# Performance work log

Hardware: AMD Instinct MI355X
Metric: run time of the kernel (lower is better)

Reference implementation:

```python
import jax, jax.numpy as jnp
import numpy as np

N, E, F_IN, EDIM, H = 50000, 1600000, 128, 16, 4
C1, C2, G, NCLS = 32, 8, 64, 10
NEG_SLOPE = 0.2


def setup_inputs() -> dict:
    key = jax.random.key(0)
    ks = jax.random.split(key, 20)
    s = 0.1
    inp = {
        "x": jax.random.normal(ks[0], (N, F_IN), jnp.float32),
        "edge_index": jax.random.randint(ks[1], (2, E), 0, N, dtype=jnp.int32),
        "edge_attr": jax.random.normal(ks[2], (E, EDIM), jnp.float32),
        "batch": jnp.sort(jax.random.randint(ks[3], (N,), 0, G, dtype=jnp.int32)),
        # layer 1 params (PyG GATConv: shared lin for src/dst, no lin bias)
        "W1": jax.random.normal(ks[4], (F_IN, H * C1), jnp.float32) * s,
        "as1": jax.random.normal(ks[5], (H, C1), jnp.float32) * s,
        "ad1": jax.random.normal(ks[6], (H, C1), jnp.float32) * s,
        "We1": jax.random.normal(ks[7], (EDIM, H * C1), jnp.float32) * s,
        "ae1": jax.random.normal(ks[8], (H, C1), jnp.float32) * s,
        "b1": jnp.zeros((H * C1,), jnp.float32),
        # layer 2 params
        "W2": jax.random.normal(ks[9], (H * C1, H * C2), jnp.float32) * s,
        "as2": jax.random.normal(ks[10], (H, C2), jnp.float32) * s,
        "ad2": jax.random.normal(ks[11], (H, C2), jnp.float32) * s,
        "We2": jax.random.normal(ks[12], (EDIM, H * C2), jnp.float32) * s,
        "ae2": jax.random.normal(ks[13], (H, C2), jnp.float32) * s,
        "b2": jnp.zeros((H * C2,), jnp.float32),
        # final linear
        "Wfc": jax.random.normal(ks[14], (H * C2, NCLS), jnp.float32) * s,
        "bfc": jnp.zeros((NCLS,), jnp.float32),
    }
    return inp


def _add_self_loops(src, dst, edge_attr):
    # PyG default: add_self_loops=True, fill_value='mean' (mean of incoming edge attrs)
    deg = jax.ops.segment_sum(jnp.ones((E,), jnp.float32), dst, num_segments=N)
    loop_attr = jax.ops.segment_sum(edge_attr, dst, num_segments=N) / jnp.maximum(deg, 1.0)[:, None]
    loop = jnp.arange(N, dtype=src.dtype)
    return (jnp.concatenate([src, loop]), jnp.concatenate([dst, loop]),
            jnp.concatenate([edge_attr, loop_attr], axis=0))


def _gat_layer(x, src, dst, ea, W, a_src, a_dst, We, a_e, b, heads, ch):
    n = x.shape[0]
    h = (x @ W).reshape(n, heads, ch)                 # [N,H,C]
    he = (ea @ We).reshape(-1, heads, ch)             # [Ef,H,C]
    al_src = jnp.einsum('nhc,hc->nh', h, a_src)       # [N,H]
    al_dst = jnp.einsum('nhc,hc->nh', h, a_dst)
    al_e = jnp.einsum('ehc,hc->eh', he, a_e)          # [Ef,H]
    alpha = al_src[src] + al_dst[dst] + al_e
    alpha = jax.nn.leaky_relu(alpha, NEG_SLOPE)
    # edge softmax grouped by destination node
    amax = jax.ops.segment_max(alpha, dst, num_segments=n)
    alpha = jnp.exp(alpha - amax[dst])
    denom = jax.ops.segment_sum(alpha, dst, num_segments=n)
    alpha = alpha / (denom[dst] + 1e-16)
    out = jax.ops.segment_sum(h[src] * alpha[..., None], dst, num_segments=n)  # [N,H,C]
    return out.reshape(n, heads * ch) + b


def reference(x, edge_index, edge_attr, batch, W1, as1, ad1, We1, ae1, b1,
              W2, as2, ad2, We2, ae2, b2, Wfc, bfc):
    src, dst = edge_index[0], edge_index[1]
    src, dst, ea = _add_self_loops(src, dst, edge_attr)
    h = jax.nn.relu(_gat_layer(x, src, dst, ea, W1, as1, ad1, We1, ae1, b1, H, C1))
    h = jax.nn.relu(_gat_layer(h, src, dst, ea, W2, as2, ad2, We2, ae2, b2, H, C2))
    # global mean pool over graphs
    cnt = jax.ops.segment_sum(jnp.ones((N,), jnp.float32), batch, num_segments=G)
    pooled = jax.ops.segment_sum(h, batch, num_segments=G) / jnp.maximum(cnt, 1.0)[:, None]
    return pooled @ Wfc + bfc
```

## Files before the change

kernel.cpp:

```cpp
#include <hip/hip_runtime.h>
#include <hip/hip_fp16.h>
#include <math.h>

typedef float4 f4;
#define NEG_SLOPE 0.2f
#define NBMAX 1024
#define BIN_CHUNK 8192

union h4pack { float2 f; __half2 h[2]; };

__global__ void k_prep(const float* __restrict__ We1, const float* __restrict__ ae1,
                       const float* __restrict__ We2, const float* __restrict__ ae2,
                       float* __restrict__ M) {
    int t = threadIdx.x;
    if (t >= 128) return;
    int sel = t >> 6, i = t & 63, d = i >> 2, h = i & 3;
    const float* W  = sel ? We2 : We1;
    const float* ae = sel ? ae2 : ae1;
    int C = sel ? 8 : 32, ncol = sel ? 32 : 128;
    float s = 0.f;
    for (int c = 0; c < C; ++c) s += W[d * ncol + h * C + c] * ae[h * C + c];
    M[sel * 64 + d * 4 + h] = s;
}

__global__ __launch_bounds__(256) void k_bhist(const int* __restrict__ ei,
                                               int* __restrict__ bcnt, int E, int NB) {
    __shared__ int hist[NBMAX];
    for (int i = threadIdx.x; i < NB; i += 256) hist[i] = 0;
    __syncthreads();
    int stride = gridDim.x * 256;
    for (int e = blockIdx.x * 256 + threadIdx.x; e < E; e += stride)
        atomicAdd(&hist[ei[E + e] >> 6], 1);
    __syncthreads();
    for (int i = threadIdx.x; i < NB; i += 256) {
        int h = hist[i];
        if (h) atomicAdd(&bcnt[i], h);
    }
}

__global__ void k_bscan(const int* __restrict__ bcnt, int* __restrict__ bprefix,
                        int* __restrict__ bcursor, int NB) {
    __shared__ int ts[NBMAX];
    int t = threadIdx.x;
    ts[t] = (t < NB) ? bcnt[t] : 0;
    __syncthreads();
    for (int off = 1; off < 1024; off <<= 1) {
        int v = (t >= off) ? ts[t - off] : 0;
        __syncthreads();
        ts[t] += v;
        __syncthreads();
    }
    int excl = (t == 0) ? 0 : ts[t - 1];
    if (t <= NB) {
        bprefix[t] = excl;
        if (t < NB) bcursor[t] = excl;
    }
}

__global__ void k_ale_lin(const float* __restrict__ ea, const float* __restrict__ Mbuf,
                          __half* __restrict__ ale1_e, __half* __restrict__ ale2_e, int E) {
    __shared__ float Ms[128];
    if (threadIdx.x < 128) Ms[threadIdx.x] = Mbuf[threadIdx.x];
    __syncthreads();
    int e = blockIdx.x * 256 + threadIdx.x;
    if (e >= E) return;
    const f4* row = (const f4*)(ea + (size_t)e * 16);
    f4 r0 = row[0], r1 = row[1], r2 = row[2], r3 = row[3];
    float a[16] = { r0.x, r0.y, r0.z, r0.w, r1.x, r1.y, r1.z, r1.w,
                    r2.x, r2.y, r2.z, r2.w, r3.x, r3.y, r3.z, r3.w };
    float s10 = 0.f, s11 = 0.f, s12 = 0.f, s13 = 0.f;
    float s20 = 0.f, s21 = 0.f, s22 = 0.f, s23 = 0.f;
#pragma unroll
    for (int dd = 0; dd < 16; ++dd) {
        float av = a[dd];
        s10 += av * Ms[dd * 4 + 0]; s11 += av * Ms[dd * 4 + 1];
        s12 += av * Ms[dd * 4 + 2]; s13 += av * Ms[dd * 4 + 3];
        s20 += av * Ms[64 + dd * 4 + 0]; s21 += av * Ms[64 + dd * 4 + 1];
        s22 += av * Ms[64 + dd * 4 + 2]; s23 += av * Ms[64 + dd * 4 + 3];
    }
    h4pack p1, p2;
    p1.h[0] = __floats2half2_rn(s10, s11); p1.h[1] = __floats2half2_rn(s12, s13);
    p2.h[0] = __floats2half2_rn(s20, s21); p2.h[1] = __floats2half2_rn(s22, s23);
    ((float2*)ale1_e)[e] = p1.f;
    ((float2*)ale2_e)[e] = p2.f;
}

__global__ __launch_bounds__(256) void k_bin(const int* __restrict__ ei,
                                             int* __restrict__ bcursor,
                                             int2* __restrict__ binned, int E, int NB) {
    __shared__ int hist[NBMAX], base[NBMAX], cur[NBMAX];
    for (int i = threadIdx.x; i < NB; i += 256) { hist[i] = 0; cur[i] = 0; }
    __syncthreads();
    int e0 = blockIdx.x * BIN_CHUNK;
    int e1 = min(e0 + BIN_CHUNK, E);
    for (int e = e0 + threadIdx.x; e < e1; e += 256)
        atomicAdd(&hist[ei[E + e] >> 6], 1);
    __syncthreads();
    for (int i = threadIdx.x; i < NB; i += 256) {
        int h = hist[i];
        if (h) base[i] = atomicAdd(&bcursor[i], h);
    }
    __syncthreads();
    for (int e = e0 + threadIdx.x; e < e1; e += 256) {
        int sr = ei[e], d = ei[E + e];
        int b = d >> 6;
        int loc = base[b] + atomicAdd(&cur[b], 1);
        binned[loc] = make_int2(sr, ((d & 63) << 26) | e);
    }
}

__global__ __launch_bounds__(256) void k_csr(const int2* __restrict__ binned,
                                             const float2* __restrict__ ale1_e,
                                             const float2* __restrict__ ale2_e,
                                             const int* __restrict__ bprefix,
                                             int* __restrict__ offsets,
                                             int* __restrict__ csr_src,
                                             float2* __restrict__ csr_ale1,
                                             float2* __restrict__ csr_ale2,
                                             int N, int E, int NB) {
    __shared__ int nhist[64], noff[65];
    int b = blockIdx.x;
    if (threadIdx.x < 64) nhist[threadIdx.x] = 0;
    __syncthreads();
    int lo = bprefix[b], hi = bprefix[b + 1];
    for (int s = lo + threadIdx.x; s < hi; s += 256)
        atomicAdd(&nhist[(binned[s].y >> 26) & 63], 1);
    __syncthreads();
    if (threadIdx.x == 0) {
        int run = 0;
        for (int i = 0; i < 64; ++i) { noff[i] = run; run += nhist[i]; }
        noff[64] = run;
    }
    __syncthreads();
    int nlo = b << 6;
    int nbn = min(64, N - nlo);
    if (threadIdx.x < nbn) offsets[nlo + threadIdx.x] = lo + noff[threadIdx.x];
    if (b == NB - 1 && threadIdx.x == 0) offsets[N] = E;
    if (threadIdx.x < 64) nhist[threadIdx.x] = 0;
    __syncthreads();
    for (int s = lo + threadIdx.x; s < hi; s += 256) {
        int2 r = binned[s];
        int dl = (r.y >> 26) & 63;
        int eid = r.y & 0x03FFFFFF;
        float2 a1 = ale1_e[eid];
        float2 a2 = ale2_e[eid];
        int slot = lo + noff[dl] + atomicAdd(&nhist[dl], 1);
        csr_src[slot] = r.x;
        csr_ale1[slot] = a1;
        csr_ale2[slot] = a2;
    }
}

template<int NOUT, int ROWS>
__global__ __launch_bounds__(256) void k_gemm(const float* __restrict__ X,
                                              const float* __restrict__ W,
                                              __half* __restrict__ Hout, int N) {
    __shared__ __align__(16) float xs[ROWS][128];
    int row0 = blockIdx.x * ROWS;
    int tid = threadIdx.x;
    constexpr int NF4 = ROWS * 32;
    const f4* x4 = (const f4*)X;
    for (int i = tid; i < NF4; i += 256) {
        int r = i >> 5, k4 = i & 31;
        f4 v;
        if (row0 + r < N) v = x4[(size_t)(row0 + r) * 32 + k4];
        else { v.x = v.y = v.z = v.w = 0.f; }
        ((f4*)&xs[r][0])[k4] = v;
    }
    __syncthreads();
    constexpr int GRP = 256 / NOUT;
    constexpr int PR  = ROWS / GRP;
    int col = tid % NOUT, rg = tid / NOUT;
    float acc[PR];
#pragma unroll
    for (int r = 0; r < PR; ++r) acc[r] = 0.f;
    for (int k = 0; k < 128; ++k) {
        float w = W[k * NOUT + col];
#pragma unroll
        for (int r = 0; r < PR; ++r) acc[r] += xs[rg + r * GRP][k] * w;
    }
#pragma unroll
    for (int r = 0; r < PR; ++r) {
        int row = row0 + rg + r * GRP;
        if (row < N) Hout[(size_t)row * NOUT + col] = __float2half(acc[r]);
    }
}

template<int C>
__global__ void k_al(const __half* __restrict__ Hm, const float* __restrict__ as_,
                     const float* __restrict__ ad_, float* __restrict__ als,
                     float* __restrict__ ald, int N) {
    int idx = blockIdx.x * 256 + threadIdx.x;
    int n = idx >> 2, h = idx & 3;
    if (n >= N) return;
    constexpr int CH = C / 4;
    const __half2* h2p = (const __half2*)(Hm + (size_t)n * C + h * CH);
    float a = 0.f, b = 0.f;
#pragma unroll
    for (int c = 0; c < CH / 2; ++c) {
        float2 v = __half22float2(h2p[c]);
        a += v.x * as_[h * CH + 2 * c] + v.y * as_[h * CH + 2 * c + 1];
        b += v.x * ad_[h * CH + 2 * c] + v.y * ad_[h * CH + 2 * c + 1];
    }
    als[n * 4 + h] = a;
    ald[n * 4 + h] = b;
}

__global__ __launch_bounds__(256) void k_alpha_node(const float2* __restrict__ csr_ale,
                                                    __half* __restrict__ alpha_csr,
                                                    const int* __restrict__ csr_src,
                                                    const float* __restrict__ als,
                                                    const float* __restrict__ ald,
                                                    const int* __restrict__ offsets,
                                                    float* __restrict__ rden,
                                                    float* __restrict__ selfa, int N) {
    int n = (blockIdx.x * 256 + threadIdx.x) >> 6;
    int lane = threadIdx.x & 63;
    if (n >= N) return;
    int j = lane >> 2, h = lane & 3;
    int s0 = offsets[n], s1 = offsets[n + 1];
    float aldn = ald[n * 4 + h];
    float den = 0.f, asum = 0.f;
    const __half* aleh = (const __half*)csr_ale;
    for (int base = s0; base < s1; base += 16) {
        int s = base + j;
        if (s < s1) {
            int src = csr_src[s];
            float ale = __half2float(aleh[(size_t)s * 4 + h]);
            float v = als[src * 4 + h] + aldn + ale;
            v = (v > 0.f) ? v : NEG_SLOPE * v;
            float e = __expf(v);
            alpha_csr[s * 4 + h] = __float2half(e);
            den += e; asum += ale;
        }
    }
    den  += __shfl_xor(den, 4);  den  += __shfl_xor(den, 8);
    den  += __shfl_xor(den, 16); den  += __shfl_xor(den, 32);
    asum += __shfl_xor(asum, 4);  asum += __shfl_xor(asum, 8);
    asum += __shfl_xor(asum, 16); asum += __shfl_xor(asum, 32);
    if (j == 0) {
        float rdeg = 1.f / fmaxf((float)(s1 - s0), 1.f);
        float v = als[n * 4 + h] + aldn + asum * rdeg;
        v = (v > 0.f) ? v : NEG_SLOPE * v;
        float es = __expf(v);
        selfa[n * 4 + h] = es;
        rden[n * 4 + h] = 1.f / (den + es + 1e-16f);
    }
}

__global__ __launch_bounds__(256) void k_aggf128(const __half* __restrict__ h16,
                                                 const __half* __restrict__ alpha16,
                                                 const float* __restrict__ rden,
                                                 const float* __restrict__ selfa,
                                                 const int* __restrict__ offsets,
                                                 const int* __restrict__ csr_src,
                                                 const float* __restrict__ bias,
                                                 float* __restrict__ Out, int N) {
    int n = (blockIdx.x * 256 + threadIdx.x) >> 6;
    int lane = threadIdx.x & 63;
    if (n >= N) return;
    int hd = lane >> 4;
    int s0 = offsets[n], s1 = offsets[n + 1];
    const __half2* H2 = (const __half2*)h16;
    float acc0 = 0.f, acc1 = 0.f;
    int e1 = s1 - 1;
    for (int s = s0; s < s1; s += 8) {
        int srck[8]; float ak[8]; __half2 hvk[8];
#pragma unroll
        for (int k = 0; k < 8; ++k) {
            int sk = min(s + k, e1);
            srck[k] = csr_src[sk];
            ak[k] = (s + k <= e1) ? __half2float(alpha16[(size_t)sk * 4 + hd]) : 0.f;
        }
#pragma unroll
        for (int k = 0; k < 8; ++k) hvk[k] = H2[(size_t)srck[k] * 64 + lane];
#pragma unroll
        for (int k = 0; k < 8; ++k) {
            float2 f = __half22float2(hvk[k]);
            acc0 = fmaf(ak[k], f.x, acc0);
            acc1 = fmaf(ak[k], f.y, acc1);
        }
    }
    float sa = selfa[n * 4 + hd];
    float2 hn = __half22float2(H2[(size_t)n * 64 + lane]);
    acc0 = fmaf(sa, hn.x, acc0);
    acc1 = fmaf(sa, hn.y, acc1);
    float rd = rden[n * 4 + hd];
    float2 bv = ((const float2*)bias)[lane];
    float2 o;
    o.x = fmaxf(fmaf(acc0, rd, bv.x), 0.f);
    o.y = fmaxf(fmaf(acc1, rd, bv.y), 0.f);
    ((float2*)Out)[(size_t)n * 64 + lane] = o;
}

__global__ __launch_bounds__(256) void k_aggf32(const __half* __restrict__ h16,
                                                const __half* __restrict__ alpha16,
                                                const float* __restrict__ rden,
                                                const float* __restrict__ selfa,
                                                const int* __restrict__ offsets,
                                                const int* __restrict__ csr_src,
                                                const float* __restrict__ bias,
                                                float* __restrict__ Out, int N) {
    int n = (blockIdx.x * 256 + threadIdx.x) >> 6;
    int lane = threadIdx.x & 63;
    if (n >= N) return;
    int j = lane >> 4;
    int p = lane & 15;
    int hd = p >> 2;
    int s0 = offsets[n], s1 = offsets[n + 1];
    const __half2* H2 = (const __half2*)h16;
    float acc0 = 0.f, acc1 = 0.f;
    int e1 = s1 - 1;
    for (int s = s0 + j; s < s1; s += 8) {
        int sA = s;
        int sB = min(s + 4, e1);
        int srcA = csr_src[sA], srcB = csr_src[sB];
        float aA = __half2float(alpha16[(size_t)sA * 4 + hd]);
        float aB = (s + 4 <= e1) ? __half2float(alpha16[(size_t)sB * 4 + hd]) : 0.f;
        __half2 hA = H2[(size_t)srcA * 16 + p];
        __half2 hB = H2[(size_t)srcB * 16 + p];
        float2 fA = __half22float2(hA), fB = __half22float2(hB);
        acc0 = fmaf(aA, fA.x, acc0); acc1 = fmaf(aA, fA.y, acc1);
        acc0 = fmaf(aB, fB.x, acc0); acc1 = fmaf(aB, fB.y, acc1);
    }
    acc0 += __shfl_xor(acc0, 16); acc0 += __shfl_xor(acc0, 32);
    acc1 += __shfl_xor(acc1, 16); acc1 += __shfl_xor(acc1, 32);
    if (j == 0) {
        float sa = selfa[n * 4 + hd];
        float2 hn = __half22float2(H2[(size_t)n * 16 + p]);
        acc0 = fmaf(sa, hn.x, acc0);
        acc1 = fmaf(sa, hn.y, acc1);
        float rd = rden[n * 4 + hd];
        float2 bv = ((const float2*)bias)[p];
        float2 o;
        o.x = fmaxf(fmaf(acc0, rd, bv.x), 0.f);
        o.y = fmaxf(fmaf(acc1, rd, bv.y), 0.f);
        ((float2*)Out)[(size_t)n * 16 + p] = o;
    }
}

__global__ void k_gbound(const int* __restrict__ batch, int* __restrict__ gstart, int N, int G) {
    int g = threadIdx.x;
    if (g > G) return;
    int lo = 0, hi = N;
    while (lo < hi) {
        int mid = (lo + hi) >> 1;
        if (batch[mid] < g) lo = mid + 1; else hi = mid;
    }
    gstart[g] = lo;
}

__global__ __launch_bounds__(256) void k_pool_grp(const float* __restrict__ out2,
                                                  const int* __restrict__ gstart,
                                                  float* __restrict__ pooled, int G) {
    __shared__ float red[8][32];
    int g = blockIdx.x;
    int t = threadIdx.x, c = t & 31, r = t >> 5;
    int s0 = gstart[g], s1 = gstart[g + 1];
    float acc = 0.f;
    for (int n = s0 + r; n < s1; n += 8) acc += out2[(size_t)n * 32 + c];
    red[r][c] = acc;
    __syncthreads();
    if (r == 0) {
        float s = red[0][c];
#pragma unroll
        for (int i = 1; i < 8; ++i) s += red[i][c];
        pooled[g * 32 + c] = s;
    }
}

__global__ void k_final(const float* __restrict__ pooled, const int* __restrict__ gstart,
                        const float* __restrict__ Wfc, const float* __restrict__ bfc,
                        float* __restrict__ out) {
    int t = threadIdx.x;
    if (t >= 640) return;
    int g = t / 10, cls = t % 10;
    float rc = 1.f / fmaxf((float)(gstart[g + 1] - gstart[g]), 1.f);
    float acc = bfc[cls];
    for (int c = 0; c < 32; ++c) acc += pooled[g * 32 + c] * rc * Wfc[c * 10 + cls];
    out[g * 10 + cls] = acc;
}

extern "C" void kernel_launch(void* const* d_in, const int* in_sizes, int n_in,
                              void* d_out, int out_size, void* d_ws, size_t ws_size,
                              hipStream_t stream) {
    const float* x    = (const float*)d_in[0];
    const int*   ei   = (const int*)  d_in[1];
    const float* ea   = (const float*)d_in[2];
    const int*   batch= (const int*)  d_in[3];
    const float* W1   = (const float*)d_in[4];
    const float* as1  = (const float*)d_in[5];
    const float* ad1  = (const float*)d_in[6];
    const float* We1  = (const float*)d_in[7];
    const float* ae1  = (const float*)d_in[8];
    const float* b1   = (const float*)d_in[9];
    const float* W2   = (const float*)d_in[10];
    const float* as2  = (const float*)d_in[11];
    const float* ad2  = (const float*)d_in[12];
    const float* We2  = (const float*)d_in[13];
    const float* ae2  = (const float*)d_in[14];
    const float* b2   = (const float*)d_in[15];
    const float* Wfc  = (const float*)d_in[16];
    const float* bfc  = (const float*)d_in[17];
    float* out = (float*)d_out;

    const int N  = in_sizes[3];
    const int E  = in_sizes[1] / 2;
    const int G  = 64;
    const int NB = (N + 63) >> 6;

    char* w = (char*)d_ws;
    size_t off = 0;
    auto alloc = [&](size_t bytes) -> void* {
        void* p = w + off;
        off = (off + bytes + 255) & ~(size_t)255;
        return p;
    };
    int*    bcnt       = (int*)   alloc((size_t)NBMAX * 4);
    int*    bprefix    = (int*)   alloc((size_t)(NBMAX + 1) * 4);
    int*    bcursor    = (int*)   alloc((size_t)NBMAX * 4);
    int*    offsets    = (int*)   alloc((size_t)(N + 1) * 4);
    int2*   binned     = (int2*)  alloc((size_t)E * 8);
    __half* ale1_e     = (__half*)alloc((size_t)E * 4 * 2);
    __half* ale2_e     = (__half*)alloc((size_t)E * 4 * 2);
    int*    csr_src    = (int*)   alloc((size_t)E * 4);
    float2* csr_ale1   = (float2*)alloc((size_t)E * 8);
    float2* csr_ale2   = (float2*)alloc((size_t)E * 8);
    float*  Mbuf       = (float*) alloc(128 * 4);
    __half* h16        = (__half*)alloc((size_t)N * 128 * 2);
    float*  out1       = (float*) alloc((size_t)N * 128 * 4);
    float*  als        = (float*) alloc((size_t)N * 4 * 4);
    float*  ald        = (float*) alloc((size_t)N * 4 * 4);
    float*  rden       = (float*) alloc((size_t)N * 4 * 4);
    float*  selfa      = (float*) alloc((size_t)N * 4 * 4);
    int*    gstart     = (int*)   alloc((G + 1) * 4);
    float*  pooled     = (float*) alloc(G * 32 * 4);
    __half* alpha_csr  = (__half*)binned;
    float*  out2 = out1;

    const int eb  = (E + 255) / 256;
    const int nb4 = (N + 3) / 4;

    hipMemsetAsync(bcnt, 0, (size_t)NBMAX * 4, stream);

    k_prep<<<1, 128, 0, stream>>>(We1, ae1, We2, ae2, Mbuf);
    k_bhist<<<128, 256, 0, stream>>>(ei, bcnt, E, NB);
    k_bscan<<<1, 1024, 0, stream>>>(bcnt, bprefix, bcursor, NB);
    k_ale_lin<<<eb, 256, 0, stream>>>(ea, Mbuf, ale1_e, ale2_e, E);
    k_bin<<<(E + BIN_CHUNK - 1) / BIN_CHUNK, 256, 0, stream>>>(ei, bcursor, binned, E, NB);
    k_csr<<<NB, 256, 0, stream>>>(binned, (const float2*)ale1_e, (const float2*)ale2_e,
                                  bprefix, offsets, csr_src, csr_ale1, csr_ale2, N, E, NB);
    k_gbound<<<1, 128, 0, stream>>>(batch, gstart, N, G);

    k_gemm<128, 16><<<(N + 15) / 16, 256, 0, stream>>>(x, W1, h16, N);
    k_al<128><<<(N * 4 + 255) / 256, 256, 0, stream>>>(h16, as1, ad1, als, ald, N);
    k_alpha_node<<<nb4, 256, 0, stream>>>(csr_ale1, alpha_csr, csr_src, als, ald, offsets, rden, selfa, N);
    k_aggf128<<<nb4, 256, 0, stream>>>(h16, alpha_csr, rden, selfa, offsets, csr_src, b1, out1, N);

    k_gemm<32, 64><<<(N + 63) / 64, 256, 0, stream>>>(out1, W2, h16, N);
    k_al<32><<<(N * 4 + 255) / 256, 256, 0, stream>>>(h16, as2, ad2, als, ald, N);
    k_alpha_node<<<nb4, 256, 0, stream>>>(csr_ale2, alpha_csr, csr_src, als, ald, offsets, rden, selfa, N);
    k_aggf32<<<nb4, 256, 0, stream>>>(h16, alpha_csr, rden, selfa, offsets, csr_src, b2, out2, N);

    k_pool_grp<<<G, 256, 0, stream>>>(out2, gstart, pooled, G);
    k_final<<<1, 640, 0, stream>>>(pooled, gstart, Wfc, bfc, out);
}
```

Before: 426.6 us.

## Store edge ids in CSR instead of permuted ale; nontemporal loads in aggregation

The CSR build no longer gathers and writes two permuted per-edge attention arrays. It stores the original edge id per CSR slot, and the alpha kernels gather ale through that id instead. Streaming loads of csr_src and alpha in the alpha and aggregation kernels become nontemporal loads, presumably to keep the h16 feature gathers in cache. The f128 aggregation loop is cut from an 8-way to a 4-way batch of loads, trading some memory-level parallelism for fewer live registers. The cost is that the ale reads become random gathers in both alpha passes instead of sequential reads.

```diff
diff --git a/kernel.cpp b/kernel.cpp
--- a/kernel.cpp
+++ b/kernel.cpp
@@ -8,6 +8,12 @@
 #define BIN_CHUNK 8192
 
 union h4pack { float2 f; __half2 h[2]; };
+
+__device__ __forceinline__ float ld_alpha_nt(const __half* p, size_t idx) {
+    unsigned short u = __builtin_nontemporal_load((const unsigned short*)p + idx);
+    __half_raw hr; hr.x = u;
+    return __half2float((__half)hr);
+}
 
 __global__ void k_prep(const float* __restrict__ We1, const float* __restrict__ ae1,
                        const float* __restrict__ We2, const float* __restrict__ ae2,
@@ -110,13 +116,10 @@
 }
 
 __global__ __launch_bounds__(256) void k_csr(const int2* __restrict__ binned,
-                                             const float2* __restrict__ ale1_e,
-                                             const float2* __restrict__ ale2_e,
                                              const int* __restrict__ bprefix,
                                              int* __restrict__ offsets,
                                              int* __restrict__ csr_src,
-                                             float2* __restrict__ csr_ale1,
-                                             float2* __restrict__ csr_ale2,
+                                             int* __restrict__ csr_eid,
                                              int N, int E, int NB) {
     __shared__ int nhist[64], noff[65];
     int b = blockIdx.x;
@@ -141,13 +144,9 @@
     for (int s = lo + threadIdx.x; s < hi; s += 256) {
         int2 r = binned[s];
         int dl = (r.y >> 26) & 63;
-        int eid = r.y & 0x03FFFFFF;
-        float2 a1 = ale1_e[eid];
-        float2 a2 = ale2_e[eid];
         int slot = lo + noff[dl] + atomicAdd(&nhist[dl], 1);
         csr_src[slot] = r.x;
-        csr_ale1[slot] = a1;
-        csr_ale2[slot] = a2;
+        csr_eid[slot] = r.y & 0x03FFFFFF;
     }
 }
 
@@ -206,9 +205,10 @@
     ald[n * 4 + h] = b;
 }
 
-__global__ __launch_bounds__(256) void k_alpha_node(const float2* __restrict__ csr_ale,
+__global__ __launch_bounds__(256) void k_alpha_node(const __half* __restrict__ ale_e,
                                                     __half* __restrict__ alpha_csr,
                                                     const int* __restrict__ csr_src,
+                                                    const int* __restrict__ csr_eid,
                                                     const float* __restrict__ als,
                                                     const float* __restrict__ ald,
                                                     const int* __restrict__ offsets,
@@ -221,12 +221,12 @@
     int s0 = offsets[n], s1 = offsets[n + 1];
     float aldn = ald[n * 4 + h];
     float den = 0.f, asum = 0.f;
-    const __half* aleh = (const __half*)csr_ale;
     for (int base = s0; base < s1; base += 16) {
         int s = base + j;
         if (s < s1) {
-            int src = csr_src[s];
-            float ale = __half2float(aleh[(size_t)s * 4 + h]);
+            int src = __builtin_nontemporal_load(csr_src + s);
+            int eid = __builtin_nontemporal_load(csr_eid + s);
+            float ale = __half2float(ale_e[(size_t)eid * 4 + h]);
             float v = als[src * 4 + h] + aldn + ale;
             v = (v > 0.f) ? v : NEG_SLOPE * v;
             float e = __expf(v);
@@ -264,22 +264,27 @@
     const __half2* H2 = (const __half2*)h16;
     float acc0 = 0.f, acc1 = 0.f;
     int e1 = s1 - 1;
-    for (int s = s0; s < s1; s += 8) {
-        int srck[8]; float ak[8]; __half2 hvk[8];
-#pragma unroll
-        for (int k = 0; k < 8; ++k) {
-            int sk = min(s + k, e1);
-            srck[k] = csr_src[sk];
-            ak[k] = (s + k <= e1) ? __half2float(alpha16[(size_t)sk * 4 + hd]) : 0.f;
-        }
-#pragma unroll
-        for (int k = 0; k < 8; ++k) hvk[k] = H2[(size_t)srck[k] * 64 + lane];
-#pragma unroll
-        for (int k = 0; k < 8; ++k) {
-            float2 f = __half22float2(hvk[k]);
-            acc0 = fmaf(ak[k], f.x, acc0);
-            acc1 = fmaf(ak[k], f.y, acc1);
-        }
+    for (int s = s0; s < s1; s += 4) {
+        int sA = s;
+        int sB = min(s + 1, e1), sC = min(s + 2, e1), sD = min(s + 3, e1);
+        int srcA = __builtin_nontemporal_load(csr_src + sA);
+        int srcB = __builtin_nontemporal_load(csr_src + sB);
+        int srcC = __builtin_nontemporal_load(csr_src + sC);
+        int srcD = __builtin_nontemporal_load(csr_src + sD);
+        float aA = ld_alpha_nt(alpha16, (size_t)sA * 4 + hd);
+        float aB = (s + 1 <= e1) ? ld_alpha_nt(alpha16, (size_t)sB * 4 + hd) : 0.f;
+        float aC = (s + 2 <= e1) ? ld_alpha_nt(alpha16, (size_t)sC * 4 + hd) : 0.f;
+        float aD = (s + 3 <= e1) ? ld_alpha_nt(alpha16, (size_t)sD * 4 + hd) : 0.f;
+        __half2 hA = H2[(size_t)srcA * 64 + lane];
+        __half2 hB = H2[(size_t)srcB * 64 + lane];
+        __half2 hC = H2[(size_t)srcC * 64 + lane];
+        __half2 hD = H2[(size_t)srcD * 64 + lane];
+        float2 fA = __half22float2(hA), fB = __half22float2(hB);
+        float2 fC = __half22float2(hC), fD = __half22float2(hD);
+        acc0 = fmaf(aA, fA.x, acc0); acc1 = fmaf(aA, fA.y, acc1);
+        acc0 = fmaf(aB, fB.x, acc0); acc1 = fmaf(aB, fB.y, acc1);
+        acc0 = fmaf(aC, fC.x, acc0); acc1 = fmaf(aC, fC.y, acc1);
+        acc0 = fmaf(aD, fD.x, acc0); acc1 = fmaf(aD, fD.y, acc1);
     }
     float sa = selfa[n * 4 + hd];
     float2 hn = __half22float2(H2[(size_t)n * 64 + lane]);
@@ -314,9 +319,10 @@
     for (int s = s0 + j; s < s1; s += 8) {
         int sA = s;
         int sB = min(s + 4, e1);
-        int srcA = csr_src[sA], srcB = csr_src[sB];
-        float aA = __half2float(alpha16[(size_t)sA * 4 + hd]);
-        float aB = (s + 4 <= e1) ? __half2float(alpha16[(size_t)sB * 4 + hd]) : 0.f;
+        int srcA = __builtin_nontemporal_load(csr_src + sA);
+        int srcB = __builtin_nontemporal_load(csr_src + sB);
+        float aA = ld_alpha_nt(alpha16, (size_t)sA * 4 + hd);
+        float aB = (s + 4 <= e1) ? ld_alpha_nt(alpha16, (size_t)sB * 4 + hd) : 0.f;
         __half2 hA = H2[(size_t)srcA * 16 + p];
         __half2 hB = H2[(size_t)srcB * 16 + p];
         float2 fA = __half22float2(hA), fB = __half22float2(hB);
@@ -424,8 +430,7 @@
     __half* ale1_e     = (__half*)alloc((size_t)E * 4 * 2);
     __half* ale2_e     = (__half*)alloc((size_t)E * 4 * 2);
     int*    csr_src    = (int*)   alloc((size_t)E * 4);
-    float2* csr_ale1   = (float2*)alloc((size_t)E * 8);
-    float2* csr_ale2   = (float2*)alloc((size_t)E * 8);
+    int*    csr_eid    = (int*)   alloc((size_t)E * 4);
     float*  Mbuf       = (float*) alloc(128 * 4);
     __half* h16        = (__half*)alloc((size_t)N * 128 * 2);
     float*  out1       = (float*) alloc((size_t)N * 128 * 4);
@@ -448,18 +453,17 @@
     k_bscan<<<1, 1024, 0, stream>>>(bcnt, bprefix, bcursor, NB);
     k_ale_lin<<<eb, 256, 0, stream>>>(ea, Mbuf, ale1_e, ale2_e, E);
     k_bin<<<(E + BIN_CHUNK - 1) / BIN_CHUNK, 256, 0, stream>>>(ei, bcursor, binned, E, NB);
-    k_csr<<<NB, 256, 0, stream>>>(binned, (const float2*)ale1_e, (const float2*)ale2_e,
-                                  bprefix, offsets, csr_src, csr_ale1, csr_ale2, N, E, NB);
+    k_csr<<<NB, 256, 0, stream>>>(binned, bprefix, offsets, csr_src, csr_eid, N, E, NB);
     k_gbound<<<1, 128, 0, stream>>>(batch, gstart, N, G);
 
     k_gemm<128, 16><<<(N + 15) / 16, 256, 0, stream>>>(x, W1, h16, N);
     k_al<128><<<(N * 4 + 255) / 256, 256, 0, stream>>>(h16, as1, ad1, als, ald, N);
-    k_alpha_node<<<nb4, 256, 0, stream>>>(csr_ale1, alpha_csr, csr_src, als, ald, offsets, rden, selfa, N);
+    k_alpha_node<<<nb4, 256, 0, stream>>>(ale1_e, alpha_csr, csr_src, csr_eid, als, ald, offsets, rden, selfa, N);
     k_aggf128<<<nb4, 256, 0, stream>>>(h16, alpha_csr, rden, selfa, offsets, csr_src, b1, out1, N);
 
     k_gemm<32, 64><<<(N + 63) / 64, 256, 0, stream>>>(out1, W2, h16, N);
     k_al<32><<<(N * 4 + 255) / 256, 256, 0, stream>>>(h16, as2, ad2, als, ald, N);
-    k_alpha_node<<<nb4, 256, 0, stream>>>(csr_ale2, alpha_csr, csr_src, als, ald, offsets, rden, selfa, N);
+    k_alpha_node<<<nb4, 256, 0, stream>>>(ale2_e, alpha_csr, csr_src, csr_eid, als, ald, offsets, rden, selfa, N);
     k_aggf32<<<nb4, 256, 0, stream>>>(h16, alpha_csr, rden, selfa, offsets, csr_src, b2, out2, N);
 
     k_pool_grp<<<G, 256, 0, stream>>>(out2, gstart, pooled, G);
```

New measurement: 447.0 us. 4.8% more time.
